# Optimization experiments

Measured on AMD Instinct MI355X. Metric: run time of the kernel, lower is better.

## Reference

```python
import jax, jax.numpy as jnp
import numpy as np

B, N, D, H, DH, M = 4, 4096, 1024, 16, 64, 256
EPS = 1e-4


def softmax_kernel(data, P, is_query):
    # data: [b,h,n,dh], P: [m,dh]  (FAVOR+ positive softmax features)
    dn = data.shape[-1] ** -0.25
    ratio = P.shape[0] ** -0.5
    dd = jnp.einsum('bhnd,md->bhnm', dn * data, P)
    diag = (jnp.sum(data * data, axis=-1) * 0.5 * dn * dn)[..., None]  # [b,h,n,1]
    if is_query:
        mx = jnp.max(dd, axis=-1, keepdims=True)  # per-query max
    else:
        mx = jnp.max(dd)  # global max (as in torch source)
    return ratio * (jnp.exp(dd - diag - mx) + EPS)


def setup_inputs() -> dict:
    key = jax.random.key(0)
    ks = jax.random.split(key, 6)
    s = 1.0 / np.sqrt(D).astype(np.float32)
    x = jax.random.normal(ks[0], (B, N, D), jnp.float32)
    Wq = jax.random.normal(ks[1], (D, H * DH), jnp.float32) * s
    Wk = jax.random.normal(ks[2], (D, H * DH), jnp.float32) * s
    Wv = jax.random.normal(ks[3], (D, H * DH), jnp.float32) * s
    Wo = jax.random.normal(ks[4], (H * DH, D), jnp.float32) * s
    bo = jnp.zeros((D,), jnp.float32)
    P = jax.random.normal(ks[5], (M, DH), jnp.float32)  # gaussian (orthogonal) projection
    return {'x': x, 'Wq': Wq, 'Wk': Wk, 'Wv': Wv, 'Wo': Wo, 'bo': bo, 'P': P}


def reference(x, Wq, Wk, Wv, Wo, bo, P):
    b, n, _ = x.shape
    # qkv projections, split heads: b n (h d) -> b h n d
    def proj(W):
        return (x @ W).reshape(b, n, H, DH).transpose(0, 2, 1, 3)
    q, k, v = proj(Wq), proj(Wk), proj(Wv)
    qp = softmax_kernel(q, P, is_query=True)   # [b,h,n,m]
    kp = softmax_kernel(k, P, is_query=False)  # [b,h,n,m]
    # linear attention (Performer)
    k_cumsum = kp.sum(axis=-2)                                   # [b,h,m]
    D_inv = 1.0 / jnp.einsum('bhnm,bhm->bhn', qp, k_cumsum)      # [b,h,n]
    ctx = jnp.einsum('bhnm,bhne->bhme', kp, v)                   # [b,h,m,dh]
    out = jnp.einsum('bhme,bhnm,bhn->bhne', ctx, qp, D_inv)      # [b,h,n,dh]
    out = out.transpose(0, 2, 1, 3).reshape(b, n, H * DH)
    return out @ Wo + bo
```

## Files before the change

### kernel.cpp

```cpp
#include <hip/hip_runtime.h>
#include <math.h>

#define NB 4
#define NSEQ 4096
#define DM 1024
#define NHEAD 16
#define DHD 64
#define MF 256
#define ROWS 16384

#define DN 0.35355339059327373f
#define RATIO 0.0625f
#define HALF_DN2 0.0625f
#define EPSF 1.0e-4f
#define THR_DEFER 4.0f

typedef __attribute__((ext_vector_type(4))) float f32x4;
typedef __attribute__((ext_vector_type(8))) short short8;
typedef __attribute__((ext_vector_type(4))) short short4v;
typedef __attribute__((ext_vector_type(8))) __bf16 bf16x8;
typedef unsigned short ushort_t;

__device__ __forceinline__ unsigned short f2bf(float f) {
  unsigned int u = __builtin_bit_cast(unsigned int, f);
  u += 0x7FFFu + ((u >> 16) & 1u);
  return (unsigned short)(u >> 16);
}
__device__ __forceinline__ float bf2f(unsigned short h) {
  unsigned int u = ((unsigned int)h) << 16;
  return __builtin_bit_cast(float, u);
}

__device__ __forceinline__ f32x4 mfma16(short8 a, short8 b, f32x4 c) {
  return __builtin_amdgcn_mfma_f32_16x16x32_bf16(
      __builtin_bit_cast(bf16x8, a), __builtin_bit_cast(bf16x8, b), c, 0, 0, 0);
}

__device__ __forceinline__ f32x4 mfma16x16(short4v a, short4v b, f32x4 c) {
#if __has_builtin(__builtin_amdgcn_mfma_f32_16x16x16bf16_1k)
  return __builtin_amdgcn_mfma_f32_16x16x16bf16_1k(a, b, c, 0, 0, 0);
#elif __has_builtin(__builtin_amdgcn_mfma_f32_16x16x16_bf16)
  typedef __attribute__((ext_vector_type(4))) __bf16 bf16x4;
  return __builtin_amdgcn_mfma_f32_16x16x16_bf16(
      __builtin_bit_cast(bf16x4, a), __builtin_bit_cast(bf16x4, b), c, 0, 0, 0);
#else
  asm volatile("s_nop 1\n\t"
               "v_mfma_f32_16x16x16_bf16 %0, %1, %2, %0\n\t"
               "s_nop 7"
               : "+v"(c) : "v"(a), "v"(b));
  return c;
#endif
}

__device__ __forceinline__ void glds16(const void* g, void* l) {
  __builtin_amdgcn_global_load_lds(
      (const __attribute__((address_space(1))) unsigned int*)g,
      (__attribute__((address_space(3))) unsigned int*)l, 16, 0, 0);
}

__global__ __launch_bounds__(256) void wtrans(const float* __restrict__ W,
                                              ushort_t* __restrict__ Wt)
{
  __shared__ float ts[64][68];
  const int tid = threadIdx.x;
  const int k0 = blockIdx.y * 64, n0 = blockIdx.x * 64;
  const int r = tid >> 4, c4 = (tid & 15) * 4;
  #pragma unroll
  for (int i = 0; i < 4; ++i) {
    float4 v = *(const float4*)&W[(size_t)(k0 + r + i * 16) * DM + n0 + c4];
    *(float4*)&ts[r + i * 16][c4] = v;
  }
  __syncthreads();
  #pragma unroll
  for (int i = 0; i < 4; ++i) {
    const int n = r + i * 16;
    ushort4 o;
    o.x = f2bf(ts[c4 + 0][n]); o.y = f2bf(ts[c4 + 1][n]);
    o.z = f2bf(ts[c4 + 2][n]); o.w = f2bf(ts[c4 + 3][n]);
    *(ushort4*)&Wt[(size_t)(n0 + n) * DM + k0 + c4] = o;
  }
}

__global__ __launch_bounds__(256) void psplit(const float* __restrict__ P,
                                              ushort_t* __restrict__ PHI,
                                              ushort_t* __restrict__ PLO)
{
  const int i = blockIdx.x * 256 + threadIdx.x;
  const float v = P[i];
  const unsigned short h = f2bf(v);
  PHI[i] = h;
  PLO[i] = f2bf(v - bf2f(h));
}

__global__ __launch_bounds__(256) void xconv(const float* __restrict__ x,
                                             ushort_t* __restrict__ xb)
{
  const size_t i = ((size_t)blockIdx.x * 256 + threadIdx.x) * 8;
  const float4 a = *(const float4*)&x[i];
  const float4 c = *(const float4*)&x[i + 4];
  short8 o;
  o[0] = f2bf(a.x); o[1] = f2bf(a.y); o[2] = f2bf(a.z); o[3] = f2bf(a.w);
  o[4] = f2bf(c.x); o[5] = f2bf(c.y); o[6] = f2bf(c.z); o[7] = f2bf(c.w);
  *(short8*)&xb[i] = o;
}

template<int EPI>
__global__ __launch_bounds__(256) void gemm_k(const ushort_t* __restrict__ Ab,
                                              const ushort_t* __restrict__ Bt,
                                              const float* __restrict__ bias,
                                              float* __restrict__ C,
                                              ushort_t* __restrict__ VT,
                                              ushort_t* __restrict__ OHL,
                                              float* __restrict__ DIAG)
{
  constexpr int K = DM, N = DM;
  __shared__ ushort_t As[128 * 32];
  __shared__ ushort_t Bs[128 * 32];

  const int tid = threadIdx.x;
  const int l = tid & 63, w = tid >> 6;
  const int ll = l & 15, lh = l >> 4;
  const int wr = w >> 1, wc = w & 1;

  const int bid = blockIdx.x;
  const int swz = (bid & 7) * ((int)gridDim.x >> 3) + (bid >> 3);
  const int bm = swz >> 3, bn = swz & 7;
  const int row0 = bm * 128, col0 = bn * 128;

  const int pb0 = w * 128 + l, pb1 = pb0 + 64;
  const int brow0 = pb0 >> 2, bkq0 = (pb0 & 3) ^ ((brow0 >> 1) & 3);
  const int brow1 = pb1 >> 2, bkq1 = (pb1 & 3) ^ ((brow1 >> 1) & 3);
  const ushort_t* bsrc0 = Bt + (size_t)(col0 + brow0) * K + bkq0 * 8;
  const ushort_t* bsrc1 = Bt + (size_t)(col0 + brow1) * K + bkq1 * 8;
  ushort_t* bdst0 = &Bs[(size_t)(w * 128) * 8];
  ushort_t* bdst1 = &Bs[(size_t)(w * 128 + 64) * 8];

  const ushort_t* asrc0 = Ab + (size_t)(row0 + brow0) * K + bkq0 * 8;
  const ushort_t* asrc1 = Ab + (size_t)(row0 + brow1) * K + bkq1 * 8;

  int aoff[4], boff[4];
  #pragma unroll
  for (int mt = 0; mt < 4; ++mt) {
    const int r = wr * 64 + mt * 16 + ll;
    aoff[mt] = (r * 4 + (lh ^ ((r >> 1) & 3))) * 8;
  }
  #pragma unroll
  for (int nt = 0; nt < 4; ++nt) {
    const int r = wc * 64 + nt * 16 + ll;
    boff[nt] = (r * 4 + (lh ^ ((r >> 1) & 3))) * 8;
  }

  f32x4 acc[4][4];
  #pragma unroll
  for (int i = 0; i < 4; ++i)
    #pragma unroll
    for (int j = 0; j < 4; ++j) acc[i][j] = (f32x4){0.f, 0.f, 0.f, 0.f};

  for (int k0 = 0; k0 < K; k0 += 32) {
    __syncthreads();
    glds16(asrc0 + k0, &As[(size_t)(w * 128) * 8]);
    glds16(asrc1 + k0, &As[(size_t)(w * 128 + 64) * 8]);
    glds16(bsrc0 + k0, bdst0);
    glds16(bsrc1 + k0, bdst1);
    __syncthreads();

    short8 av[4], bv[4];
    #pragma unroll
    for (int mt = 0; mt < 4; ++mt) av[mt] = *(const short8*)&As[aoff[mt]];
    #pragma unroll
    for (int nt = 0; nt < 4; ++nt) bv[nt] = *(const short8*)&Bs[boff[nt]];
    #pragma unroll
    for (int mt = 0; mt < 4; ++mt)
      #pragma unroll
      for (int nt = 0; nt < 4; ++nt)
        acc[mt][nt] = mfma16(av[mt], bv[nt], acc[mt][nt]);
  }

  if constexpr (EPI == 1) {
    #pragma unroll
    for (int mt = 0; mt < 4; ++mt) {
      #pragma unroll
      for (int nt = 0; nt < 4; ++nt) {
        const int row = row0 + wr * 64 + mt * 16 + lh * 4;
        const int col = col0 + wc * 64 + nt * 16 + ll;
        const float bv_ = bias[col];
        #pragma unroll
        for (int j = 0; j < 4; ++j)
          C[(size_t)(row + j) * N + col] = acc[mt][nt][j] + bv_;
      }
    }
  } else if constexpr (EPI == 2) {
    #pragma unroll
    for (int mt = 0; mt < 4; ++mt) {
      #pragma unroll
      for (int nt = 0; nt < 4; ++nt) {
        const int rg = row0 + wr * 64 + mt * 16 + lh * 4;
        const int cg = col0 + wc * 64 + nt * 16 + ll;
        const int b = rg >> 12, n = rg & 4095;
        const int h = cg >> 6, dh = cg & 63;
        ushort4 o;
        o.x = f2bf(acc[mt][nt][0]); o.y = f2bf(acc[mt][nt][1]);
        o.z = f2bf(acc[mt][nt][2]); o.w = f2bf(acc[mt][nt][3]);
        *(ushort4*)&VT[(((size_t)b * 16 + h) * 64 + dh) * 4096 + n] = o;
      }
    }
  } else {
    const int hglob = (col0 >> 6) + wc;
    #pragma unroll
    for (int mt = 0; mt < 4; ++mt) {
      float rssq[4] = {0.f, 0.f, 0.f, 0.f};
      #pragma unroll
      for (int nt = 0; nt < 4; ++nt) {
        const int row = row0 + wr * 64 + mt * 16 + lh * 4;
        const int e = nt * 16 + ll;
        #pragma unroll
        for (int j = 0; j < 4; ++j) {
          const float v = acc[mt][nt][j];
          rssq[j] += v * v;
          const unsigned short hh = f2bf(v);
          const size_t base = ((size_t)(row + j) * 16 + hglob) * 128 + e;
          OHL[base] = hh;
          OHL[base + 64] = f2bf(v - bf2f(hh));
        }
      }
      #pragma unroll
      for (int j = 0; j < 4; ++j) {
        float s = rssq[j];
        s += __shfl_xor(s, 1, 64); s += __shfl_xor(s, 2, 64);
        s += __shfl_xor(s, 4, 64); s += __shfl_xor(s, 8, 64);
        if (ll == 0) {
          const int row = row0 + wr * 64 + mt * 16 + lh * 4 + j;
          DIAG[(((row >> 12) * 16 + hglob) << 12) + (row & 4095)] = HALF_DN2 * s;
        }
      }
    }
  }
}

__global__ __launch_bounds__(256) void kside8(const ushort_t* __restrict__ KHL,
                                              const ushort_t* __restrict__ VT,
                                              const ushort_t* __restrict__ PHI,
                                              const ushort_t* __restrict__ PLO,
                                              const float* __restrict__ DIAGK,
                                              ushort_t* __restrict__ partC,
                                              float* __restrict__ partK,
                                              float* __restrict__ mw,
                                              float* __restrict__ vsum,
                                              unsigned* __restrict__ mxp)
{
  const int tid = threadIdx.x;
  const int l = tid & 63, mg = tid >> 6;
  const int ll = l & 15, lh = l >> 4;
  const int blk = blockIdx.x;
  const int bh = blk >> 4, ck = blk & 15;
  const int b = bh >> 4, h = bh & 15;

  short8 pfh[4][2], pfl[4][2];
  #pragma unroll
  for (int mt = 0; mt < 4; ++mt)
    #pragma unroll
    for (int ks = 0; ks < 2; ++ks) {
      const size_t off = (size_t)(mg * 64 + mt * 16 + ll) * 64 + ks * 32 + lh * 8;
      pfh[mt][ks] = *(const short8*)&PHI[off];
      pfl[mt][ks] = *(const short8*)&PLO[off];
    }

  f32x4 apv[4][4];
  #pragma unroll
  for (int i = 0; i < 4; ++i)
    #pragma unroll
    for (int j = 0; j < 4; ++j) apv[i][j] = (f32x4){0.f, 0.f, 0.f, 0.f};
  float kcp[4] = {0.f, 0.f, 0.f, 0.f};
  float vs[4] = {0.f, 0.f, 0.f, 0.f};
  float m_run = -1.0e30f, tmax = -1.0e30f;

  const int n0 = ck * 256;
  const ushort_t* krow = KHL + ((size_t)(b * NSEQ + n0 + ll) * 16 + h) * 128 + lh * 8;
  const ushort_t* vrow = VT + (size_t)bh * 64 * NSEQ + n0 + lh * 4;
  const float* drow = DIAGK + bh * 4096 + n0 + lh * 4;

  short8 kh0 = *(const short8*)(krow);
  short8 kh1 = *(const short8*)(krow + 32);
  short8 kl0 = *(const short8*)(krow + 64);
  short8 kl1 = *(const short8*)(krow + 96);

  for (int it = 0; it < 16; ++it) {
    const int itn = (it < 15) ? it + 1 : 15;
    const ushort_t* kpn = krow + (size_t)itn * 16 * 2048;
    const short8 nh0 = *(const short8*)(kpn);
    const short8 nh1 = *(const short8*)(kpn + 32);
    const short8 nl0 = *(const short8*)(kpn + 64);
    const short8 nl1 = *(const short8*)(kpn + 96);

    const float4 dg4 = *(const float4*)(drow + it * 16);
    short4v vf[4];
    #pragma unroll
    for (int dt = 0; dt < 4; ++dt)
      vf[dt] = *(const short4v*)&vrow[(size_t)(dt * 16 + ll) * NSEQ + it * 16];

    f32x4 dda[4];
    #pragma unroll
    for (int mt = 0; mt < 4; ++mt) {
      f32x4 acc = (f32x4){0.f, 0.f, 0.f, 0.f};
      acc = mfma16(kh0, pfh[mt][0], acc); acc = mfma16(kh1, pfh[mt][1], acc);
      acc = mfma16(kh0, pfl[mt][0], acc); acc = mfma16(kh1, pfl[mt][1], acc);
      acc = mfma16(kl0, pfh[mt][0], acc); acc = mfma16(kl1, pfh[mt][1], acc);
      #pragma unroll
      for (int jr = 0; jr < 4; ++jr) acc[jr] *= DN;
      dda[mt] = acc;
    }

    float pm = -1.0e30f;
    #pragma unroll
    for (int mt = 0; mt < 4; ++mt)
      #pragma unroll
      for (int jr = 0; jr < 4; ++jr) pm = fmaxf(pm, dda[mt][jr]);
    tmax = fmaxf(tmax, pm);
    if (!__all(pm <= m_run + THR_DEFER)) {
      float pw = fmaxf(pm, m_run);
      pw = fmaxf(pw, __shfl_xor(pw, 1, 64));  pw = fmaxf(pw, __shfl_xor(pw, 2, 64));
      pw = fmaxf(pw, __shfl_xor(pw, 4, 64));  pw = fmaxf(pw, __shfl_xor(pw, 8, 64));
      pw = fmaxf(pw, __shfl_xor(pw, 16, 64)); pw = fmaxf(pw, __shfl_xor(pw, 32, 64));
      const float sc = __expf(m_run - pw);
      #pragma unroll
      for (int mt = 0; mt < 4; ++mt) {
        kcp[mt] *= sc;
        #pragma unroll
        for (int dt = 0; dt < 4; ++dt) apv[mt][dt] *= sc;
      }
      m_run = pw;
    }

    const float dgv[4] = {dg4.x, dg4.y, dg4.z, dg4.w};
    short4v qa[4];
    #pragma unroll
    for (int mt = 0; mt < 4; ++mt) {
      short4v o;
      float s = 0.f;
      #pragma unroll
      for (int jr = 0; jr < 4; ++jr) {
        const float kv = __expf(dda[mt][jr] - dgv[jr] - m_run);
        const unsigned short ub = f2bf(kv);
        o[jr] = (short)ub;
        s += bf2f(ub);
      }
      qa[mt] = o;
      kcp[mt] += s;
    }

    if (mg == 0) {
      #pragma unroll
      for (int dt = 0; dt < 4; ++dt)
        #pragma unroll
        for (int e = 0; e < 4; ++e) vs[dt] += bf2f((ushort_t)vf[dt][e]);
    }

    #pragma unroll
    for (int dt = 0; dt < 4; ++dt)
      #pragma unroll
      for (int mt = 0; mt < 4; ++mt)
        apv[mt][dt] = mfma16x16(qa[mt], vf[dt], apv[mt][dt]);

    kh0 = nh0; kh1 = nh1; kl0 = nl0; kl1 = nl1;
  }

  #pragma unroll
  for (int mt = 0; mt < 4; ++mt) {
    float s = kcp[mt];
    s += __shfl_xor(s, 16, 64);
    s += __shfl_xor(s, 32, 64);
    if (lh == 0) partK[blk * 256 + mg * 64 + mt * 16 + ll] = s;
  }
  #pragma unroll
  for (int mt = 0; mt < 4; ++mt)
    #pragma unroll
    for (int dt = 0; dt < 4; ++dt)
      #pragma unroll
      for (int jr = 0; jr < 4; ++jr) {
        const int m = mg * 64 + mt * 16 + lh * 4 + jr;
        const int dh = dt * 16 + ll;
        partC[(size_t)blk * 16384 + (size_t)m * 64 + dh] = f2bf(apv[mt][dt][jr]);
      }
  if (mg == 0) {
    #pragma unroll
    for (int dt = 0; dt < 4; ++dt) {
      float s = vs[dt];
      s += __shfl_xor(s, 16, 64);
      s += __shfl_xor(s, 32, 64);
      if (lh == 0) atomicAdd(&vsum[bh * 64 + dt * 16 + ll], s);
    }
  }
  tmax = fmaxf(tmax, __shfl_xor(tmax, 1, 64));  tmax = fmaxf(tmax, __shfl_xor(tmax, 2, 64));
  tmax = fmaxf(tmax, __shfl_xor(tmax, 4, 64));  tmax = fmaxf(tmax, __shfl_xor(tmax, 8, 64));
  tmax = fmaxf(tmax, __shfl_xor(tmax, 16, 64)); tmax = fmaxf(tmax, __shfl_xor(tmax, 32, 64));
  if (l == 0) {
    atomicMax(mxp, __float_as_uint(tmax));
    mw[blk * 4 + mg] = m_run;
  }
}

__global__ __launch_bounds__(256) void combine4(const ushort_t* __restrict__ partC,
                                                const float* __restrict__ partK,
                                                const float* __restrict__ mw,
                                                const float* __restrict__ vsum,
                                                const unsigned* __restrict__ mxp,
                                                float* __restrict__ KCS,
                                                ushort_t* __restrict__ CTH,
                                                ushort_t* __restrict__ CTL)
{
  const int tid = threadIdx.x;
  const int bh = blockIdx.x >> 2, mc = blockIdx.x & 3;
  const float MX = __uint_as_float(*mxp);
  float s[16];
  #pragma unroll
  for (int c = 0; c < 16; ++c)
    s[c] = RATIO * __expf(mw[(bh * 16 + c) * 4 + mc] - MX);

  __shared__ float ts[64][68];
  const int r = tid >> 4, c4 = (tid & 15) * 4;
  const float reps = RATIO * EPSF;
  const float4 v4 = *(const float4*)&vsum[bh * 64 + c4];
  #pragma unroll
  for (int i = 0; i < 4; ++i) {
    const int ml = r + i * 16;
    const int m = mc * 64 + ml;
    float4 a;
    a.x = reps * v4.x; a.y = reps * v4.y; a.z = reps * v4.z; a.w = reps * v4.w;
    #pragma unroll
    for (int c = 0; c < 16; ++c) {
      const ushort4 p = *(const ushort4*)&partC[(size_t)(bh * 16 + c) * 16384 +
                                                (size_t)m * 64 + c4];
      a.x += s[c] * bf2f(p.x); a.y += s[c] * bf2f(p.y);
      a.z += s[c] * bf2f(p.z); a.w += s[c] * bf2f(p.w);
    }
    *(float4*)&ts[ml][c4] = a;
  }
  if (tid < 64) {
    const int m = mc * 64 + tid;
    float kv = reps * 4096.0f;
    #pragma unroll
    for (int c = 0; c < 16; ++c) kv += s[c] * partK[(bh * 16 + c) * 256 + m];
    KCS[bh * 256 + m] = kv;
  }
  __syncthreads();
  #pragma unroll
  for (int i = 0; i < 4; ++i) {
    const int dh = r + i * 16;
    ushort4 oh, ol;
    #pragma unroll
    for (int k = 0; k < 4; ++k) {
      const float v = ts[c4 + k][dh];
      const unsigned short hh = f2bf(v);
      ((unsigned short*)&oh)[k] = hh;
      ((unsigned short*)&ol)[k] = f2bf(v - bf2f(hh));
    }
    const size_t o = ((size_t)bh * 64 + dh) * MF + mc * 64 + c4;
    *(ushort4*)&CTH[o] = oh;
    *(ushort4*)&CTL[o] = ol;
  }
}

__global__ __launch_bounds__(512, 2) void qside6(const ushort_t* __restrict__ QHL,
                                                 const ushort_t* __restrict__ PHI,
                                                 const ushort_t* __restrict__ PLO,
                                                 const float* __restrict__ DIAGQ,
                                                 const float* __restrict__ kcs,
                                                 const ushort_t* __restrict__ CTH,
                                                 const ushort_t* __restrict__ CTL,
                                                 ushort_t* __restrict__ attb)
{
  extern __shared__ ushort_t lds[];
  ushort_t* pst = lds;
  ushort_t* ctf = lds + 32768;
  ushort_t* kcf = lds + 65536;

  const int tid = threadIdx.x;
  const int l = tid & 63, w = tid >> 6;
  const int ll = l & 15, lh = l >> 4;
  const int bh = blockIdx.x >> 4, qt = blockIdx.x & 15;
  const int b = bh >> 4, h = bh & 15;

  #pragma unroll
  for (int i = 0; i < 8; ++i) {
    const int f = tid + i * 512;
    const int fl = f & 63, r = f >> 6;
    const int p = r & 1, ks = (r >> 1) & 1, mt = r >> 2;
    const ushort_t* src = (p ? PLO : PHI) + (mt * 16 + (fl & 15)) * 64 + ks * 32 + (fl >> 4) * 8;
    *(short8*)&pst[f * 8] = *(const short8*)src;
  }
  #pragma unroll
  for (int i = 0; i < 16; ++i) {
    const int g = tid + i * 512;
    const int gl = g & 63, r = g >> 6;
    const int dt = r & 3, r2 = r >> 2, mt = r2 & 15, p = r2 >> 4;
    const ushort_t* src = (p ? CTL : CTH) +
        ((size_t)bh * 64 + dt * 16 + (gl & 15)) * MF + mt * 16 + (gl >> 4) * 4;
    *(ushort4*)&ctf[g * 4] = *(const ushort4*)src;
  }
  #pragma unroll
  for (int i = 0; i < 2; ++i) {
    const int u = tid + i * 512;
    const int ul = u & 63, mt = u >> 6;
    const int cll = ul & 15, clh = ul >> 4;
    ushort4 o = make_ushort4(0, 0, 0, 0);
    if (cll < 2) {
      #pragma unroll
      for (int e = 0; e < 4; ++e) {
        const float kv = kcs[bh * MF + mt * 16 + clh * 4 + e];
        const unsigned short hi = f2bf(kv);
        ((ushort_t*)&o)[e] = (cll == 0) ? hi : f2bf(kv - bf2f(hi));
      }
    }
    *(ushort4*)&kcf[u * 4] = o;
  }
  __syncthreads();

  const int nloc0 = qt * 256 + w * 32;
  const int rowb0 = b * NSEQ + nloc0;

  short8 qh0[2], ql0[2], qh1[2], ql1[2];
  #pragma unroll
  for (int ks = 0; ks < 2; ++ks) {
    const size_t base = ((size_t)(rowb0 + ll) * 16 + h) * 128 + ks * 32 + lh * 8;
    qh0[ks] = *(const short8*)&QHL[base];
    ql0[ks] = *(const short8*)&QHL[base + 64];
    qh1[ks] = *(const short8*)&QHL[base + (size_t)16 * 2048];
    ql1[ks] = *(const short8*)&QHL[base + (size_t)16 * 2048 + 64];
  }
  const float dg0 = DIAGQ[bh * 4096 + nloc0 + ll];
  const float dg1 = DIAGQ[bh * 4096 + nloc0 + 16 + ll];

  f32x4 dd0[16], dd1[16];
  #pragma unroll
  for (int mt = 0; mt < 16; ++mt) {
    const short8 ph0 = *(const short8*)&pst[((mt * 2 + 0) * 2 + 0) * 512 + l * 8];
    const short8 ph1 = *(const short8*)&pst[((mt * 2 + 1) * 2 + 0) * 512 + l * 8];
    const short8 pl0 = *(const short8*)&pst[((mt * 2 + 0) * 2 + 1) * 512 + l * 8];
    const short8 pl1 = *(const short8*)&pst[((mt * 2 + 1) * 2 + 1) * 512 + l * 8];
    f32x4 a0 = (f32x4){0.f, 0.f, 0.f, 0.f};
    f32x4 a1 = (f32x4){0.f, 0.f, 0.f, 0.f};
    a0 = mfma16(ph0, qh0[0], a0); a0 = mfma16(ph1, qh0[1], a0);
    a0 = mfma16(ph0, ql0[0], a0); a0 = mfma16(ph1, ql0[1], a0);
    a0 = mfma16(pl0, qh0[0], a0); a0 = mfma16(pl1, qh0[1], a0);
    a1 = mfma16(ph0, qh1[0], a1); a1 = mfma16(ph1, qh1[1], a1);
    a1 = mfma16(ph0, ql1[0], a1); a1 = mfma16(ph1, ql1[1], a1);
    a1 = mfma16(pl0, qh1[0], a1); a1 = mfma16(pl1, qh1[1], a1);
    dd0[mt] = a0; dd1[mt] = a1;
  }

  float rm0 = -3.0e38f, rm1 = -3.0e38f;
  #pragma unroll
  for (int mt = 0; mt < 16; ++mt) {
    rm0 = fmaxf(rm0, fmaxf(fmaxf(dd0[mt][0], dd0[mt][1]), fmaxf(dd0[mt][2], dd0[mt][3])));
    rm1 = fmaxf(rm1, fmaxf(fmaxf(dd1[mt][0], dd1[mt][1]), fmaxf(dd1[mt][2], dd1[mt][3])));
  }
  rm0 = fmaxf(rm0, __shfl_xor(rm0, 16, 64)); rm0 = fmaxf(rm0, __shfl_xor(rm0, 32, 64));
  rm1 = fmaxf(rm1, __shfl_xor(rm1, 16, 64)); rm1 = fmaxf(rm1, __shfl_xor(rm1, 32, 64));
  rm0 *= DN; rm1 *= DN;

  short4v qp0[16], qp1[16];
  #pragma unroll
  for (int mt = 0; mt < 16; ++mt) {
    short4v o0, o1;
    #pragma unroll
    for (int jr = 0; jr < 4; ++jr) {
      o0[jr] = (short)f2bf(RATIO * (__expf(dd0[mt][jr] * DN - dg0 - rm0) + EPSF));
      o1[jr] = (short)f2bf(RATIO * (__expf(dd1[mt][jr] * DN - dg1 - rm1) + EPSF));
    }
    qp0[mt] = o0; qp1[mt] = o1;
  }

  f32x4 av0[4], av1[4];
  #pragma unroll
  for (int dt = 0; dt < 4; ++dt) {
    av0[dt] = (f32x4){0.f, 0.f, 0.f, 0.f};
    av1[dt] = (f32x4){0.f, 0.f, 0.f, 0.f};
  }
  f32x4 aK0 = (f32x4){0.f, 0.f, 0.f, 0.f};
  f32x4 aK1 = (f32x4){0.f, 0.f, 0.f, 0.f};
  #pragma unroll
  for (int mt = 0; mt < 16; ++mt) {
    const short4v kcv = *(const short4v*)&kcf[mt * 256 + l * 4];
    aK0 = mfma16x16(qp0[mt], kcv, aK0);
    aK1 = mfma16x16(qp1[mt], kcv, aK1);
    #pragma unroll
    for (int dt = 0; dt < 4; ++dt) {
      const short4v ch = *(const short4v*)&ctf[((0 * 16 + mt) * 4 + dt) * 256 + l * 4];
      const short4v cl = *(const short4v*)&ctf[((16 + mt) * 4 + dt) * 256 + l * 4];
      av0[dt] = mfma16x16(qp0[mt], ch, av0[dt]);
      av0[dt] = mfma16x16(qp0[mt], cl, av0[dt]);
      av1[dt] = mfma16x16(qp1[mt], ch, av1[dt]);
      av1[dt] = mfma16x16(qp1[mt], cl, av1[dt]);
    }
  }

  float di0[4], di1[4];
  #pragma unroll
  for (int jr = 0; jr < 4; ++jr) {
    const float h0 = __shfl(aK0[jr], (l & 48), 64);
    const float l0 = __shfl(aK0[jr], (l & 48) | 1, 64);
    const float h1 = __shfl(aK1[jr], (l & 48), 64);
    const float l1 = __shfl(aK1[jr], (l & 48) | 1, 64);
    di0[jr] = 1.0f / (h0 + l0);
    di1[jr] = 1.0f / (h1 + l1);
  }

  #pragma unroll
  for (int dt = 0; dt < 4; ++dt)
    #pragma unroll
    for (int jr = 0; jr < 4; ++jr) {
      const int col = h * DHD + dt * 16 + ll;
      attb[(size_t)(rowb0 + lh * 4 + jr) * DM + col] = f2bf(av0[dt][jr] * di0[jr]);
      attb[(size_t)(rowb0 + 16 + lh * 4 + jr) * DM + col] = f2bf(av1[dt][jr] * di1[jr]);
    }
}

extern "C" void kernel_launch(void* const* d_in, const int* in_sizes, int n_in,
                              void* d_out, int out_size, void* d_ws, size_t ws_size,
                              hipStream_t stream)
{
  const float* x  = (const float*)d_in[0];
  const float* Wq = (const float*)d_in[1];
  const float* Wk = (const float*)d_in[2];
  const float* Wv = (const float*)d_in[3];
  const float* Wo = (const float*)d_in[4];
  const float* bo = (const float*)d_in[5];
  const float* P  = (const float*)d_in[6];
  float* out = (float*)d_out;

  char* wp = (char*)d_ws;
  ushort_t* QHL   = (ushort_t*)(wp + 0);
  ushort_t* KHL   = (ushort_t*)(wp + 67108864);
  ushort_t* VT    = (ushort_t*)(wp + 134217728);
  ushort_t* Wqt   = (ushort_t*)(wp + 167772160);
  ushort_t* Wkt   = (ushort_t*)(wp + 169869312);
  ushort_t* Wvt   = (ushort_t*)(wp + 171966464);
  ushort_t* Wot   = (ushort_t*)(wp + 174063616);
  ushort_t* PHI   = (ushort_t*)(wp + 176160768);
  ushort_t* PLO   = (ushort_t*)(wp + 176193536);
  float*    DIAGQ = (float*)(wp + 176226304);
  float*    DIAGK = (float*)(wp + 177274880);
  float*    PARTK = (float*)(wp + 178323456);
  float*    MW    = (float*)(wp + 179372032);
  float*    VSUM  = (float*)(wp + 179388416);
  unsigned* MX    = (unsigned*)(wp + 179404800);
  float*    KCS   = (float*)(wp + 179405056);
  ushort_t* CTH   = (ushort_t*)(wp + 179470592);
  ushort_t* CTL   = (ushort_t*)(wp + 181567744);
  ushort_t* ATTB  = KHL;

  ushort_t* PARTC = (ushort_t*)d_out;
  ushort_t* XB    = (ushort_t*)((char*)d_out + 33554432);

  dim3 tg(16, 16);
  wtrans<<<tg, 256, 0, stream>>>(Wq, Wqt);
  wtrans<<<tg, 256, 0, stream>>>(Wk, Wkt);
  wtrans<<<tg, 256, 0, stream>>>(Wv, Wvt);
  wtrans<<<tg, 256, 0, stream>>>(Wo, Wot);
  psplit<<<64, 256, 0, stream>>>(P, PHI, PLO);
  xconv<<<8192, 256, 0, stream>>>(x, XB);
  hipMemsetAsync(VSUM, 0, 16640, stream);

  gemm_k<3><<<1024, 256, 0, stream>>>(XB, Wqt, nullptr, nullptr, nullptr, QHL, DIAGQ);
  gemm_k<3><<<1024, 256, 0, stream>>>(XB, Wkt, nullptr, nullptr, nullptr, KHL, DIAGK);
  gemm_k<2><<<1024, 256, 0, stream>>>(XB, Wvt, nullptr, nullptr, VT, nullptr, nullptr);

  kside8<<<1024, 256, 0, stream>>>(KHL, VT, PHI, PLO, DIAGK, PARTC, PARTK, MW, VSUM, MX);
  combine4<<<256, 256, 0, stream>>>(PARTC, PARTK, MW, VSUM, MX, KCS, CTH, CTL);
  qside6<<<1024, 512, 139264, stream>>>(QHL, PHI, PLO, DIAGQ, KCS, CTH, CTL, ATTB);

  gemm_k<1><<<1024, 256, 0, stream>>>(ATTB, Wot, bo, out, nullptr, nullptr, nullptr);
}
```

Measured before the change: 445.6 us.

## Process two 16-row key tiles per iteration in kside with fewer, larger chunks

The key-side kernel now handles 512 sequence positions per block instead of 256 and processes two 16-row tiles per loop iteration, halving the grid to 512 blocks and setting a minimum-occupancy launch bound. Partial context sums are stored as fp32 instead of bf16, and the combine kernel reduces over 8 chunks instead of 16. This cuts per-block setup and combine traffic and gives each wave more independent MFMA work, at the cost of more registers, fewer blocks for latency hiding, and wider partial-sum writes.

```diff
diff --git a/kernel.cpp b/kernel.cpp
--- a/kernel.cpp
+++ b/kernel.cpp
@@ -237,22 +237,22 @@
   }
 }
 
-__global__ __launch_bounds__(256) void kside8(const ushort_t* __restrict__ KHL,
-                                              const ushort_t* __restrict__ VT,
-                                              const ushort_t* __restrict__ PHI,
-                                              const ushort_t* __restrict__ PLO,
-                                              const float* __restrict__ DIAGK,
-                                              ushort_t* __restrict__ partC,
-                                              float* __restrict__ partK,
-                                              float* __restrict__ mw,
-                                              float* __restrict__ vsum,
-                                              unsigned* __restrict__ mxp)
+__global__ __launch_bounds__(256, 2) void kside5w(const ushort_t* __restrict__ KHL,
+                                                  const ushort_t* __restrict__ VT,
+                                                  const ushort_t* __restrict__ PHI,
+                                                  const ushort_t* __restrict__ PLO,
+                                                  const float* __restrict__ DIAGK,
+                                                  float* __restrict__ partC,
+                                                  float* __restrict__ partK,
+                                                  float* __restrict__ mw,
+                                                  float* __restrict__ vsum,
+                                                  unsigned* __restrict__ mxp)
 {
   const int tid = threadIdx.x;
   const int l = tid & 63, mg = tid >> 6;
   const int ll = l & 15, lh = l >> 4;
   const int blk = blockIdx.x;
-  const int bh = blk >> 4, ck = blk & 15;
+  const int bh = blk >> 3, ck = blk & 7;
   const int b = bh >> 4, h = bh & 15;
 
   short8 pfh[4][2], pfl[4][2];
@@ -274,47 +274,60 @@
   float vs[4] = {0.f, 0.f, 0.f, 0.f};
   float m_run = -1.0e30f, tmax = -1.0e30f;
 
-  const int n0 = ck * 256;
+  const int n0 = ck * 512;
   const ushort_t* krow = KHL + ((size_t)(b * NSEQ + n0 + ll) * 16 + h) * 128 + lh * 8;
   const ushort_t* vrow = VT + (size_t)bh * 64 * NSEQ + n0 + lh * 4;
   const float* drow = DIAGK + bh * 4096 + n0 + lh * 4;
 
-  short8 kh0 = *(const short8*)(krow);
-  short8 kh1 = *(const short8*)(krow + 32);
-  short8 kl0 = *(const short8*)(krow + 64);
-  short8 kl1 = *(const short8*)(krow + 96);
+  short8 kA[4], kB[4];
+  #pragma unroll
+  for (int q = 0; q < 4; ++q) {
+    kA[q] = *(const short8*)(krow + q * 32);
+    kB[q] = *(const short8*)(krow + 16 * 2048 + q * 32);
+  }
 
   for (int it = 0; it < 16; ++it) {
     const int itn = (it < 15) ? it + 1 : 15;
-    const ushort_t* kpn = krow + (size_t)itn * 16 * 2048;
-    const short8 nh0 = *(const short8*)(kpn);
-    const short8 nh1 = *(const short8*)(kpn + 32);
-    const short8 nl0 = *(const short8*)(kpn + 64);
-    const short8 nl1 = *(const short8*)(kpn + 96);
-
-    const float4 dg4 = *(const float4*)(drow + it * 16);
-    short4v vf[4];
-    #pragma unroll
-    for (int dt = 0; dt < 4; ++dt)
-      vf[dt] = *(const short4v*)&vrow[(size_t)(dt * 16 + ll) * NSEQ + it * 16];
-
-    f32x4 dda[4];
+    const ushort_t* kpA = krow + (size_t)itn * 32 * 2048;
+    const ushort_t* kpB = kpA + 16 * 2048;
+    short8 nA[4], nB[4];
+    #pragma unroll
+    for (int q = 0; q < 4; ++q) {
+      nA[q] = *(const short8*)(kpA + q * 32);
+      nB[q] = *(const short8*)(kpB + q * 32);
+    }
+
+    const float4 dgA = *(const float4*)(drow + it * 32);
+    const float4 dgB = *(const float4*)(drow + it * 32 + 16);
+    short4v vfA[4], vfB[4];
+    #pragma unroll
+    for (int dt = 0; dt < 4; ++dt) {
+      vfA[dt] = *(const short4v*)&vrow[(size_t)(dt * 16 + ll) * NSEQ + it * 32];
+      vfB[dt] = *(const short4v*)&vrow[(size_t)(dt * 16 + ll) * NSEQ + it * 32 + 16];
+    }
+
+    f32x4 ddA[4], ddB[4];
     #pragma unroll
     for (int mt = 0; mt < 4; ++mt) {
-      f32x4 acc = (f32x4){0.f, 0.f, 0.f, 0.f};
-      acc = mfma16(kh0, pfh[mt][0], acc); acc = mfma16(kh1, pfh[mt][1], acc);
-      acc = mfma16(kh0, pfl[mt][0], acc); acc = mfma16(kh1, pfl[mt][1], acc);
-      acc = mfma16(kl0, pfh[mt][0], acc); acc = mfma16(kl1, pfh[mt][1], acc);
-      #pragma unroll
-      for (int jr = 0; jr < 4; ++jr) acc[jr] *= DN;
-      dda[mt] = acc;
+      f32x4 a = (f32x4){0.f, 0.f, 0.f, 0.f};
+      f32x4 c = (f32x4){0.f, 0.f, 0.f, 0.f};
+      a = mfma16(kA[0], pfh[mt][0], a); a = mfma16(kA[1], pfh[mt][1], a);
+      a = mfma16(kA[0], pfl[mt][0], a); a = mfma16(kA[1], pfl[mt][1], a);
+      a = mfma16(kA[2], pfh[mt][0], a); a = mfma16(kA[3], pfh[mt][1], a);
+      c = mfma16(kB[0], pfh[mt][0], c); c = mfma16(kB[1], pfh[mt][1], c);
+      c = mfma16(kB[0], pfl[mt][0], c); c = mfma16(kB[1], pfl[mt][1], c);
+      c = mfma16(kB[2], pfh[mt][0], c); c = mfma16(kB[3], pfh[mt][1], c);
+      #pragma unroll
+      for (int jr = 0; jr < 4; ++jr) { a[jr] *= DN; c[jr] *= DN; }
+      ddA[mt] = a; ddB[mt] = c;
     }
 
     float pm = -1.0e30f;
     #pragma unroll
     for (int mt = 0; mt < 4; ++mt)
       #pragma unroll
-      for (int jr = 0; jr < 4; ++jr) pm = fmaxf(pm, dda[mt][jr]);
+      for (int jr = 0; jr < 4; ++jr)
+        pm = fmaxf(pm, fmaxf(ddA[mt][jr], ddB[mt][jr]));
     tmax = fmaxf(tmax, pm);
     if (!__all(pm <= m_run + THR_DEFER)) {
       float pw = fmaxf(pm, m_run);
@@ -331,20 +344,25 @@
       m_run = pw;
     }
 
-    const float dgv[4] = {dg4.x, dg4.y, dg4.z, dg4.w};
-    short4v qa[4];
+    const float dgvA[4] = {dgA.x, dgA.y, dgA.z, dgA.w};
+    const float dgvB[4] = {dgB.x, dgB.y, dgB.z, dgB.w};
+    short4v qaA[4], qaB[4];
     #pragma unroll
     for (int mt = 0; mt < 4; ++mt) {
-      short4v o;
+      short4v oA, oB;
       float s = 0.f;
       #pragma unroll
       for (int jr = 0; jr < 4; ++jr) {
-        const float kv = __expf(dda[mt][jr] - dgv[jr] - m_run);
-        const unsigned short ub = f2bf(kv);
-        o[jr] = (short)ub;
-        s += bf2f(ub);
-      }
-      qa[mt] = o;
+        const float kvA = __expf(ddA[mt][jr] - dgvA[jr] - m_run);
+        const float kvB = __expf(ddB[mt][jr] - dgvB[jr] - m_run);
+        const unsigned short uA = f2bf(kvA);
+        const unsigned short uB = f2bf(kvB);
+        oA[jr] = (short)uA;
+        oB[jr] = (short)uB;
+        s += bf2f(uA) + bf2f(uB);
+      }
+      qaA[mt] = oA;
+      qaB[mt] = oB;
       kcp[mt] += s;
     }
 
@@ -352,16 +370,20 @@
       #pragma unroll
       for (int dt = 0; dt < 4; ++dt)
         #pragma unroll
-        for (int e = 0; e < 4; ++e) vs[dt] += bf2f((ushort_t)vf[dt][e]);
+        for (int e = 0; e < 4; ++e)
+          vs[dt] += bf2f((ushort_t)vfA[dt][e]) + bf2f((ushort_t)vfB[dt][e]);
     }
 
     #pragma unroll
     for (int dt = 0; dt < 4; ++dt)
       #pragma unroll
-      for (int mt = 0; mt < 4; ++mt)
-        apv[mt][dt] = mfma16x16(qa[mt], vf[dt], apv[mt][dt]);
-
-    kh0 = nh0; kh1 = nh1; kl0 = nl0; kl1 = nl1;
+      for (int mt = 0; mt < 4; ++mt) {
+        apv[mt][dt] = mfma16x16(qaA[mt], vfA[dt], apv[mt][dt]);
+        apv[mt][dt] = mfma16x16(qaB[mt], vfB[dt], apv[mt][dt]);
+      }
+
+    #pragma unroll
+    for (int q = 0; q < 4; ++q) { kA[q] = nA[q]; kB[q] = nB[q]; }
   }
 
   #pragma unroll
@@ -379,7 +401,7 @@
       for (int jr = 0; jr < 4; ++jr) {
         const int m = mg * 64 + mt * 16 + lh * 4 + jr;
         const int dh = dt * 16 + ll;
-        partC[(size_t)blk * 16384 + (size_t)m * 64 + dh] = f2bf(apv[mt][dt][jr]);
+        partC[(size_t)blk * 16384 + (size_t)m * 64 + dh] = apv[mt][dt][jr];
       }
   if (mg == 0) {
     #pragma unroll
@@ -399,22 +421,22 @@
   }
 }
 
-__global__ __launch_bounds__(256) void combine4(const ushort_t* __restrict__ partC,
-                                                const float* __restrict__ partK,
-                                                const float* __restrict__ mw,
-                                                const float* __restrict__ vsum,
-                                                const unsigned* __restrict__ mxp,
-                                                float* __restrict__ KCS,
-                                                ushort_t* __restrict__ CTH,
-                                                ushort_t* __restrict__ CTL)
+__global__ __launch_bounds__(256) void combine(const float* __restrict__ partC,
+                                               const float* __restrict__ partK,
+                                               const float* __restrict__ mw,
+                                               const float* __restrict__ vsum,
+                                               const unsigned* __restrict__ mxp,
+                                               float* __restrict__ KCS,
+                                               ushort_t* __restrict__ CTH,
+                                               ushort_t* __restrict__ CTL)
 {
   const int tid = threadIdx.x;
   const int bh = blockIdx.x >> 2, mc = blockIdx.x & 3;
   const float MX = __uint_as_float(*mxp);
-  float s[16];
-  #pragma unroll
-  for (int c = 0; c < 16; ++c)
-    s[c] = RATIO * __expf(mw[(bh * 16 + c) * 4 + mc] - MX);
+  float s[8];
+  #pragma unroll
+  for (int c = 0; c < 8; ++c)
+    s[c] = RATIO * __expf(mw[(bh * 8 + c) * 4 + mc] - MX);
 
   __shared__ float ts[64][68];
   const int r = tid >> 4, c4 = (tid & 15) * 4;
@@ -423,15 +445,13 @@
   #pragma unroll
   for (int i = 0; i < 4; ++i) {
     const int ml = r + i * 16;
-    const int m = mc * 64 + ml;
     float4 a;
     a.x = reps * v4.x; a.y = reps * v4.y; a.z = reps * v4.z; a.w = reps * v4.w;
     #pragma unroll
-    for (int c = 0; c < 16; ++c) {
-      const ushort4 p = *(const ushort4*)&partC[(size_t)(bh * 16 + c) * 16384 +
-                                                (size_t)m * 64 + c4];
-      a.x += s[c] * bf2f(p.x); a.y += s[c] * bf2f(p.y);
-      a.z += s[c] * bf2f(p.z); a.w += s[c] * bf2f(p.w);
+    for (int c = 0; c < 8; ++c) {
+      const float4 p = *(const float4*)&partC[(size_t)(bh * 8 + c) * 16384 +
+                                              (size_t)(mc * 64 + ml) * 64 + c4];
+      a.x += s[c] * p.x; a.y += s[c] * p.y; a.z += s[c] * p.z; a.w += s[c] * p.w;
     }
     *(float4*)&ts[ml][c4] = a;
   }
@@ -439,7 +459,7 @@
     const int m = mc * 64 + tid;
     float kv = reps * 4096.0f;
     #pragma unroll
-    for (int c = 0; c < 16; ++c) kv += s[c] * partK[(bh * 16 + c) * 256 + m];
+    for (int c = 0; c < 8; ++c) kv += s[c] * partK[(bh * 8 + c) * 256 + m];
     KCS[bh * 256 + m] = kv;
   }
   __syncthreads();
@@ -641,15 +661,15 @@
   float*    DIAGQ = (float*)(wp + 176226304);
   float*    DIAGK = (float*)(wp + 177274880);
   float*    PARTK = (float*)(wp + 178323456);
-  float*    MW    = (float*)(wp + 179372032);
-  float*    VSUM  = (float*)(wp + 179388416);
-  unsigned* MX    = (unsigned*)(wp + 179404800);
-  float*    KCS   = (float*)(wp + 179405056);
-  ushort_t* CTH   = (ushort_t*)(wp + 179470592);
-  ushort_t* CTL   = (ushort_t*)(wp + 181567744);
+  float*    MW    = (float*)(wp + 178847744);
+  float*    VSUM  = (float*)(wp + 178855936);
+  unsigned* MX    = (unsigned*)(wp + 178872320);
+  float*    KCS   = (float*)(wp + 178872576);
+  ushort_t* CTH   = (ushort_t*)(wp + 178938112);
+  ushort_t* CTL   = (ushort_t*)(wp + 181035264);
   ushort_t* ATTB  = KHL;
 
-  ushort_t* PARTC = (ushort_t*)d_out;
+  float*    PARTC = (float*)d_out;
   ushort_t* XB    = (ushort_t*)((char*)d_out + 33554432);
 
   dim3 tg(16, 16);
@@ -659,14 +679,14 @@
   wtrans<<<tg, 256, 0, stream>>>(Wo, Wot);
   psplit<<<64, 256, 0, stream>>>(P, PHI, PLO);
   xconv<<<8192, 256, 0, stream>>>(x, XB);
-  hipMemsetAsync(VSUM, 0, 16640, stream);
+  hipMemsetAsync(VSUM, 0, 16384 + 256, stream);
 
   gemm_k<3><<<1024, 256, 0, stream>>>(XB, Wqt, nullptr, nullptr, nullptr, QHL, DIAGQ);
   gemm_k<3><<<1024, 256, 0, stream>>>(XB, Wkt, nullptr, nullptr, nullptr, KHL, DIAGK);
   gemm_k<2><<<1024, 256, 0, stream>>>(XB, Wvt, nullptr, nullptr, VT, nullptr, nullptr);
 
-  kside8<<<1024, 256, 0, stream>>>(KHL, VT, PHI, PLO, DIAGK, PARTC, PARTK, MW, VSUM, MX);
-  combine4<<<256, 256, 0, stream>>>(PARTC, PARTK, MW, VSUM, MX, KCS, CTH, CTL);
+  kside5w<<<512, 256, 0, stream>>>(KHL, VT, PHI, PLO, DIAGK, PARTC, PARTK, MW, VSUM, MX);
+  combine<<<256, 256, 0, stream>>>(PARTC, PARTK, MW, VSUM, MX, KCS, CTH, CTL);
   qside6<<<1024, 512, 139264, stream>>>(QHL, PHI, PLO, DIAGQ, KCS, CTH, CTL, ATTB);
 
   gemm_k<1><<<1024, 256, 0, stream>>>(ATTB, Wot, bo, out, nullptr, nullptr, nullptr);
```

New measurement: 450.9 us. No clear change (+1.2%).
